# Kernel optimization log

Hardware: AMD Instinct MI355X
Metric: run time of the kernel (lower is better)

Reference implementation:

```python
import jax, jax.numpy as jnp
import numpy as np

N_NODES = 100000
N_EDGES = 1600000
DIN = 128
DH = 128
EPS = 1e-5


def _gcn_conv(x, src, dst, W, b, n):
    # x: [N, F_in] -> [N, F_out]; PyG GCNConv: transform, add self-loops,
    # symmetric normalization D^-1/2 (A+I) D^-1/2, scatter-add, + bias.
    h = x @ W.T                                        # [N, F_out]
    loops = jnp.arange(n, dtype=src.dtype)
    s = jnp.concatenate([src, loops])                  # [E+N]
    d = jnp.concatenate([dst, loops])                  # [E+N]
    w = jnp.ones(s.shape[0], dtype=x.dtype)
    deg = jax.ops.segment_sum(w, d, num_segments=n)    # [N]
    dinv = jnp.where(deg > 0, jax.lax.rsqrt(deg), 0.0)
    norm = dinv[s] * dinv[d]                           # [E+N]
    msg = h[s] * norm[:, None]                         # [E+N, F_out] (big buffer)
    out = jax.ops.segment_sum(msg, d, num_segments=n)  # [N, F_out]
    return out + b


def setup_inputs() -> dict:
    key = jax.random.key(0)
    ks = jax.random.split(key, 8)
    x = jax.random.normal(ks[0], (N_NODES, DIN), dtype=jnp.float32)
    edge_index = jax.random.randint(ks[1], (2, N_EDGES), 0, N_NODES, dtype=jnp.int32)
    sc = 1.0 / np.sqrt(DIN)
    return {
        "x": x,
        "edge_index": edge_index,
        "gamma": jnp.ones((DIN,), jnp.float32),
        "beta": jnp.zeros((DIN,), jnp.float32),
        "W1": jax.random.normal(ks[2], (DH, DIN), jnp.float32) * sc,
        "b1": jnp.zeros((DH,), jnp.float32),
        "W2": jax.random.normal(ks[3], (DH, DH), jnp.float32) * (1.0 / np.sqrt(DH)),
        "b2": jnp.zeros((DH,), jnp.float32),
        "Wc1": jax.random.normal(ks[4], (16, DH), jnp.float32) * (1.0 / np.sqrt(DH)),
        "bc1": jnp.zeros((16,), jnp.float32),
        "Wc2": jax.random.normal(ks[5], (2, 16), jnp.float32) * 0.25,
        "bc2": jnp.zeros((2,), jnp.float32),
    }


def reference(x, edge_index, gamma, beta, W1, b1, W2, b2, Wc1, bc1, Wc2, bc2):
    n = x.shape[0]
    src, dst = edge_index[0], edge_index[1]
    # BatchNorm1d (training mode: batch stats, biased variance)
    mu = jnp.mean(x, axis=0)
    var = jnp.mean((x - mu) ** 2, axis=0)
    xn = (x - mu) * jax.lax.rsqrt(var + EPS) * gamma + beta
    h = jax.nn.relu(_gcn_conv(xn, src, dst, W1, b1, n))
    h = jax.nn.relu(_gcn_conv(h, src, dst, W2, b2, n))
    h = jax.nn.relu(h @ Wc1.T + bc1)
    return h @ Wc2.T + bc2  # [N, 2]
```

## Files before the change

### kernel.cpp

```cpp
#include <hip/hip_runtime.h>
#include <hip/hip_fp16.h>

#define NFEAT 128
#define EPSV 1e-5f
#define BSH 9
#define BSZ 512
#define CHUNK 8192
#define CAP 12288

typedef _Float16 h8 __attribute__((ext_vector_type(8)));
typedef float f4 __attribute__((ext_vector_type(4)));

__global__ __launch_bounds__(256) void k_stats(const float4* __restrict__ X4,
    float* __restrict__ part, int total4)
{
    int t = threadIdx.x;
    int stride = gridDim.x * 256;
    int i = blockIdx.x * 256 + t;
    float4 s = make_float4(0.f, 0.f, 0.f, 0.f);
    float4 q = make_float4(0.f, 0.f, 0.f, 0.f);
    for (; i + 3 * stride < total4; i += 4 * stride) {
        float4 a = X4[i], b = X4[i + stride], c = X4[i + 2 * stride], d = X4[i + 3 * stride];
        s.x += (a.x + b.x) + (c.x + d.x);
        s.y += (a.y + b.y) + (c.y + d.y);
        s.z += (a.z + b.z) + (c.z + d.z);
        s.w += (a.w + b.w) + (c.w + d.w);
        q.x += (a.x * a.x + b.x * b.x) + (c.x * c.x + d.x * d.x);
        q.y += (a.y * a.y + b.y * b.y) + (c.y * c.y + d.y * d.y);
        q.z += (a.z * a.z + b.z * b.z) + (c.z * c.z + d.z * d.z);
        q.w += (a.w * a.w + b.w * b.w) + (c.w * c.w + d.w * d.w);
    }
    for (; i < total4; i += stride) {
        float4 a = X4[i];
        s.x += a.x; s.y += a.y; s.z += a.z; s.w += a.w;
        q.x = fmaf(a.x, a.x, q.x); q.y = fmaf(a.y, a.y, q.y);
        q.z = fmaf(a.z, a.z, q.z); q.w = fmaf(a.w, a.w, q.w);
    }
    __shared__ float4 ls[256], lq[256];
    ls[t] = s; lq[t] = q;
    __syncthreads();
    #pragma unroll
    for (int off = 128; off >= 32; off >>= 1) {
        if (t < off) {
            float4 a = ls[t], b = ls[t + off];
            ls[t] = make_float4(a.x + b.x, a.y + b.y, a.z + b.z, a.w + b.w);
            float4 c = lq[t], d = lq[t + off];
            lq[t] = make_float4(c.x + d.x, c.y + d.y, c.z + d.z, c.w + d.w);
        }
        __syncthreads();
    }
    if (t < 32) {
        float4* p4 = (float4*)(part + blockIdx.x * 256);
        p4[t] = ls[t];
        p4[32 + t] = lq[t];
    }
}

__global__ __launch_bounds__(256) void k_stats2(const float* __restrict__ part,
    float* __restrict__ part2)
{
    int v = threadIdx.x;
    int b0 = blockIdx.x * 32;
    float s = 0.f;
    #pragma unroll 8
    for (int j = 0; j < 32; ++j) s += part[(b0 + j) * 256 + v];
    part2[blockIdx.x * 256 + v] = s;
}

__global__ __launch_bounds__(256) void k_foldW(const float* __restrict__ W1,
    const float* __restrict__ gamma, const float* __restrict__ beta,
    const float* __restrict__ part2, float invN,
    float* __restrict__ W1p, float* __restrict__ c1)
{
    int o = (blockIdx.x * 256 + threadIdx.x) >> 6;
    int l = threadIdx.x & 63;
    float part = 0.f;
    #pragma unroll
    for (int j = 0; j < 2; ++j) {
        int k = 2 * l + j;
        float sm = 0.f, sq = 0.f;
        #pragma unroll
        for (int b = 0; b < 8; ++b) {
            sm += part2[b * 256 + k];
            sq += part2[b * 256 + 128 + k];
        }
        float mu = sm * invN;
        float var = fmaf(-mu, mu, sq * invN);
        float sc = rsqrtf(var + EPSV) * gamma[k];
        float sh = fmaf(-mu, sc, beta[k]);
        float w = W1[o * NFEAT + k];
        W1p[o * NFEAT + k] = w * sc;
        part = fmaf(sh, w, part);
    }
    #pragma unroll
    for (int off = 32; off > 0; off >>= 1) part += __shfl_down(part, off);
    if (l == 0) c1[o] = part;
}

__global__ __launch_bounds__(256) void k_bucket(const int* __restrict__ src,
    const int* __restrict__ dst, int* __restrict__ bnxt,
    int* __restrict__ packed, int E, int NB)
{
    __shared__ int hist[1024];
    __shared__ int base[1024];
    int t = threadIdx.x;
    int c0 = blockIdx.x * (CHUNK / 4);
    int c1 = min(E >> 2, c0 + CHUNK / 4);
    const int4* dst4 = (const int4*)dst;
    const int4* src4 = (const int4*)src;
    for (int i = t; i < NB; i += 256) hist[i] = 0;
    __syncthreads();
    for (int e = c0 + t; e < c1; e += 256) {
        int4 d = dst4[e];
        atomicAdd(&hist[d.x >> BSH], 1);
        atomicAdd(&hist[d.y >> BSH], 1);
        atomicAdd(&hist[d.z >> BSH], 1);
        atomicAdd(&hist[d.w >> BSH], 1);
    }
    __syncthreads();
    for (int i = t; i < NB; i += 256) {
        int h = hist[i];
        base[i] = h ? atomicAdd(&bnxt[i], h) : 0;
        hist[i] = 0;
    }
    __syncthreads();
    for (int e = c0 + t; e < c1; e += 256) {
        int4 d = dst4[e];
        int4 s = src4[e];
        int b, p;
        b = d.x >> BSH; p = base[b] + atomicAdd(&hist[b], 1); packed[b * CAP + p] = (s.x << BSH) | (d.x & (BSZ - 1));
        b = d.y >> BSH; p = base[b] + atomicAdd(&hist[b], 1); packed[b * CAP + p] = (s.y << BSH) | (d.y & (BSZ - 1));
        b = d.z >> BSH; p = base[b] + atomicAdd(&hist[b], 1); packed[b * CAP + p] = (s.z << BSH) | (d.z & (BSZ - 1));
        b = d.w >> BSH; p = base[b] + atomicAdd(&hist[b], 1); packed[b * CAP + p] = (s.w << BSH) | (d.w & (BSZ - 1));
    }
    if (blockIdx.x == 0) {
        for (int e = (E & ~3) + t; e < E; e += 256) {
            int d = dst[e];
            int b = d >> BSH;
            int p = atomicAdd(&bnxt[b], 1);
            packed[b * CAP + p] = (src[e] << BSH) | (d & (BSZ - 1));
        }
    }
}

__global__ __launch_bounds__(256) void k_bscan(const int* __restrict__ bnxt,
    int* __restrict__ boff, int NB)
{
    __shared__ int ps[256];
    int t = threadIdx.x;
    int v = (t < NB) ? bnxt[t] : 0;
    ps[t] = v;
    __syncthreads();
    #pragma unroll
    for (int off = 1; off < 256; off <<= 1) {
        int u = ps[t];
        if (t >= off) u += ps[t - off];
        __syncthreads();
        ps[t] = u;
        __syncthreads();
    }
    if (t < NB) boff[t] = ps[t] - v;
    if (t == NB - 1) boff[NB] = ps[t];
}

__global__ __launch_bounds__(256) void k_bdp(const int* __restrict__ packed,
    const int* __restrict__ bnxt, const int* __restrict__ boff,
    int* __restrict__ rp, float* __restrict__ dinv,
    int* __restrict__ csr, int N, int E)
{
    __shared__ int cnt[BSZ];
    __shared__ int ps[256];
    int b = blockIdx.x, t = threadIdx.x;
    cnt[2 * t] = 0; cnt[2 * t + 1] = 0;
    __syncthreads();
    int ecnt = bnxt[b];
    const int* pk = packed + b * CAP;
    const int4* p4 = (const int4*)pk;
    int n4 = ecnt >> 2;
    for (int e = t; e < n4; e += 256) {
        int4 v = p4[e];
        atomicAdd(&cnt[v.x & (BSZ - 1)], 1);
        atomicAdd(&cnt[v.y & (BSZ - 1)], 1);
        atomicAdd(&cnt[v.z & (BSZ - 1)], 1);
        atomicAdd(&cnt[v.w & (BSZ - 1)], 1);
    }
    for (int e = (n4 << 2) + t; e < ecnt; e += 256)
        atomicAdd(&cnt[pk[e] & (BSZ - 1)], 1);
    __syncthreads();
    int v0 = cnt[2 * t], v1 = cnt[2 * t + 1];
    int ts = v0 + v1;
    ps[t] = ts;
    __syncthreads();
    #pragma unroll
    for (int off = 1; off < 256; off <<= 1) {
        int u = ps[t];
        if (t >= off) u += ps[t - off];
        __syncthreads();
        ps[t] = u;
        __syncthreads();
    }
    int gbase = boff[b] + ps[t] - ts;
    cnt[2 * t] = gbase;
    cnt[2 * t + 1] = gbase + v0;
    int nbase = b << BSH;
    if (nbase + 2 * t < N) {
        rp[nbase + 2 * t] = gbase;
        dinv[nbase + 2 * t] = rsqrtf((float)(v0 + 1));
    }
    if (nbase + 2 * t + 1 < N) {
        rp[nbase + 2 * t + 1] = gbase + v0;
        dinv[nbase + 2 * t + 1] = rsqrtf((float)(v1 + 1));
    }
    if (b == 0 && t == 0) rp[N] = E;
    __syncthreads();
    for (int e = t; e < n4; e += 256) {
        int4 v = p4[e];
        int p;
        p = atomicAdd(&cnt[v.x & (BSZ - 1)], 1); csr[p] = v.x >> BSH;
        p = atomicAdd(&cnt[v.y & (BSZ - 1)], 1); csr[p] = v.y >> BSH;
        p = atomicAdd(&cnt[v.z & (BSZ - 1)], 1); csr[p] = v.z >> BSH;
        p = atomicAdd(&cnt[v.w & (BSZ - 1)], 1); csr[p] = v.w >> BSH;
    }
    for (int e = (n4 << 2) + t; e < ecnt; e += 256) {
        int v = pk[e];
        int p = atomicAdd(&cnt[v & (BSZ - 1)], 1);
        csr[p] = v >> BSH;
    }
}

__global__ __launch_bounds__(256) void k_gemm_f32(const float4* __restrict__ X4,
    const float* __restrict__ W, const float* __restrict__ C,
    const float* __restrict__ dinv, _Float16* __restrict__ Y, int N)
{
    __shared__ _Float16 w16[NFEAT * 136];
    __shared__ _Float16 ost[4 * 16 * 136];
    const float4* W4 = (const float4*)W;
    for (int idx = threadIdx.x; idx < NFEAT * NFEAT / 4; idx += 256) {
        float4 w = W4[idx];
        int o = idx >> 5, k = (idx & 31) * 4;
        _Float16* d = &w16[o * 136 + k];
        d[0] = (_Float16)w.x; d[1] = (_Float16)w.y;
        d[2] = (_Float16)w.z; d[3] = (_Float16)w.w;
    }
    __syncthreads();

    const h8* Wv = (const h8*)w16;
    h8* Yv = (h8*)Y;
    int lane = threadIdx.x & 63;
    int lr = lane & 15;
    int lk = lane >> 4;
    _Float16* slab = ost + (threadIdx.x >> 6) * (16 * 136);
    h8* slabv = (h8*)slab;
    int wid = (blockIdx.x * blockDim.x + threadIdx.x) >> 6;
    int nw = (gridDim.x * blockDim.x) >> 6;
    int ntiles = N >> 4;

    for (int tile = wid; tile < ntiles; tile += nw) {
        int r0 = tile << 4;
        h8 a[4];
        #pragma unroll
        for (int kg = 0; kg < 4; ++kg) {
            long fi = (long)(r0 + lr) * 32 + (kg * 4 + lk) * 2;
            float4 u = X4[fi];
            float4 v = X4[fi + 1];
            a[kg][0] = (_Float16)u.x; a[kg][1] = (_Float16)u.y;
            a[kg][2] = (_Float16)u.z; a[kg][3] = (_Float16)u.w;
            a[kg][4] = (_Float16)v.x; a[kg][5] = (_Float16)v.y;
            a[kg][6] = (_Float16)v.z; a[kg][7] = (_Float16)v.w;
        }

        f4 acc[8];
        #pragma unroll
        for (int nt = 0; nt < 8; ++nt) acc[nt] = (f4)(0.f);
        #pragma unroll
        for (int nt = 0; nt < 8; ++nt) {
            int o = nt * 16 + lr;
            #pragma unroll
            for (int kg = 0; kg < 4; ++kg) {
                h8 b = Wv[o * 17 + kg * 4 + lk];
                acc[nt] = __builtin_amdgcn_mfma_f32_16x16x32_f16(a[kg], b, acc[nt], 0, 0, 0);
            }
        }

        int rbase = lk * 4;
        float dv0 = dinv[r0 + rbase + 0];
        float dv1 = dinv[r0 + rbase + 1];
        float dv2 = dinv[r0 + rbase + 2];
        float dv3 = dinv[r0 + rbase + 3];
        #pragma unroll
        for (int nt = 0; nt < 8; ++nt) {
            int c = nt * 16 + lr;
            float cb = C[c];
            slab[(rbase + 0) * 136 + c] = (_Float16)((acc[nt][0] + cb) * dv0);
            slab[(rbase + 1) * 136 + c] = (_Float16)((acc[nt][1] + cb) * dv1);
            slab[(rbase + 2) * 136 + c] = (_Float16)((acc[nt][2] + cb) * dv2);
            slab[(rbase + 3) * 136 + c] = (_Float16)((acc[nt][3] + cb) * dv3);
        }
        #pragma unroll
        for (int j = 0; j < 4; ++j) {
            int row = j * 4 + lk;
            Yv[(long)(r0 + row) * 16 + lr] = slabv[row * 17 + lr];
        }
    }
}

__global__ __launch_bounds__(256) void k_gemm_f16(const _Float16* __restrict__ X,
    const float* __restrict__ W, const float* __restrict__ dinv,
    _Float16* __restrict__ Y, int N)
{
    __shared__ _Float16 w16[NFEAT * 136];
    __shared__ _Float16 ost[4 * 16 * 136];
    const float4* W4 = (const float4*)W;
    for (int idx = threadIdx.x; idx < NFEAT * NFEAT / 4; idx += 256) {
        float4 w = W4[idx];
        int o = idx >> 5, k = (idx & 31) * 4;
        _Float16* d = &w16[o * 136 + k];
        d[0] = (_Float16)w.x; d[1] = (_Float16)w.y;
        d[2] = (_Float16)w.z; d[3] = (_Float16)w.w;
    }
    __syncthreads();

    const h8* Xv = (const h8*)X;
    const h8* Wv = (const h8*)w16;
    h8* Yv = (h8*)Y;
    int lane = threadIdx.x & 63;
    int lr = lane & 15;
    int lk = lane >> 4;
    _Float16* slab = ost + (threadIdx.x >> 6) * (16 * 136);
    h8* slabv = (h8*)slab;
    int wid = (blockIdx.x * blockDim.x + threadIdx.x) >> 6;
    int nw = (gridDim.x * blockDim.x) >> 6;
    int ntiles = N >> 4;

    for (int tile = wid; tile < ntiles; tile += nw) {
        int r0 = tile << 4;
        h8 a[4];
        #pragma unroll
        for (int kg = 0; kg < 4; ++kg)
            a[kg] = Xv[(long)(r0 + lr) * 16 + kg * 4 + lk];

        f4 acc[8];
        #pragma unroll
        for (int nt = 0; nt < 8; ++nt) acc[nt] = (f4)(0.f);
        #pragma unroll
        for (int nt = 0; nt < 8; ++nt) {
            int o = nt * 16 + lr;
            #pragma unroll
            for (int kg = 0; kg < 4; ++kg) {
                h8 b = Wv[o * 17 + kg * 4 + lk];
                acc[nt] = __builtin_amdgcn_mfma_f32_16x16x32_f16(a[kg], b, acc[nt], 0, 0, 0);
            }
        }

        int rbase = lk * 4;
        float dv0 = dinv[r0 + rbase + 0];
        float dv1 = dinv[r0 + rbase + 1];
        float dv2 = dinv[r0 + rbase + 2];
        float dv3 = dinv[r0 + rbase + 3];
        #pragma unroll
        for (int nt = 0; nt < 8; ++nt) {
            int c = nt * 16 + lr;
            slab[(rbase + 0) * 136 + c] = (_Float16)(acc[nt][0] * dv0);
            slab[(rbase + 1) * 136 + c] = (_Float16)(acc[nt][1] * dv1);
            slab[(rbase + 2) * 136 + c] = (_Float16)(acc[nt][2] * dv2);
            slab[(rbase + 3) * 136 + c] = (_Float16)(acc[nt][3] * dv3);
        }
        #pragma unroll
        for (int j = 0; j < 4; ++j) {
            int row = j * 4 + lk;
            Yv[(long)(r0 + row) * 16 + lr] = slabv[row * 17 + lr];
        }
    }
}

__global__ __launch_bounds__(256) void k_agg(const unsigned int* __restrict__ TT,
    const int* __restrict__ rp, const int* __restrict__ csr,
    const float* __restrict__ dinv, const float* __restrict__ bias,
    unsigned int* __restrict__ OUT, int N)
{
    int wid = (blockIdx.x * 256 + threadIdx.x) >> 6;
    if (wid >= N) return;
    int lane = threadIdx.x & 63;
    unsigned int sv = TT[wid * 64 + lane];
    float2 acc = __half22float2(*(const __half2*)&sv);
    int e = rp[wid], e1 = rp[wid + 1];
    for (; e + 16 <= e1; e += 16) {
        int si[16];
        #pragma unroll
        for (int j = 0; j < 16; ++j) si[j] = csr[e + j];
        unsigned int v[16];
        #pragma unroll
        for (int j = 0; j < 16; ++j) v[j] = TT[si[j] * 64 + lane];
        float ax = 0.f, ay = 0.f;
        #pragma unroll
        for (int j = 0; j < 16; ++j) {
            float2 f = __half22float2(*(const __half2*)&v[j]);
            ax += f.x; ay += f.y;
        }
        acc.x += ax; acc.y += ay;
    }
    for (; e + 8 <= e1; e += 8) {
        int s0 = csr[e + 0], s1 = csr[e + 1], s2 = csr[e + 2], s3 = csr[e + 3];
        int s4 = csr[e + 4], s5 = csr[e + 5], s6 = csr[e + 6], s7 = csr[e + 7];
        unsigned int v0 = TT[s0 * 64 + lane];
        unsigned int v1 = TT[s1 * 64 + lane];
        unsigned int v2 = TT[s2 * 64 + lane];
        unsigned int v3 = TT[s3 * 64 + lane];
        unsigned int v4 = TT[s4 * 64 + lane];
        unsigned int v5 = TT[s5 * 64 + lane];
        unsigned int v6 = TT[s6 * 64 + lane];
        unsigned int v7 = TT[s7 * 64 + lane];
        float2 f0 = __half22float2(*(const __half2*)&v0);
        float2 f1 = __half22float2(*(const __half2*)&v1);
        float2 f2 = __half22float2(*(const __half2*)&v2);
        float2 f3 = __half22float2(*(const __half2*)&v3);
        float2 f4_ = __half22float2(*(const __half2*)&v4);
        float2 f5 = __half22float2(*(const __half2*)&v5);
        float2 f6 = __half22float2(*(const __half2*)&v6);
        float2 f7 = __half22float2(*(const __half2*)&v7);
        acc.x += ((f0.x + f1.x) + (f2.x + f3.x)) + ((f4_.x + f5.x) + (f6.x + f7.x));
        acc.y += ((f0.y + f1.y) + (f2.y + f3.y)) + ((f4_.y + f5.y) + (f6.y + f7.y));
    }
    for (; e < e1; ++e) {
        int s = csr[e];
        unsigned int v = TT[s * 64 + lane];
        float2 f = __half22float2(*(const __half2*)&v);
        acc.x += f.x; acc.y += f.y;
    }
    float dv = dinv[wid];
    float ox = fmaxf(fmaf(acc.x, dv, bias[lane * 2 + 0]), 0.f);
    float oy = fmaxf(fmaf(acc.y, dv, bias[lane * 2 + 1]), 0.f);
    __half2 o2 = __floats2half2_rn(ox, oy);
    OUT[wid * 64 + lane] = *(unsigned int*)&o2;
}

__global__ __launch_bounds__(256) void k_head(const __half* __restrict__ H,
    const float* __restrict__ Wc1, const float* __restrict__ bc1,
    const float* __restrict__ Wc2, const float* __restrict__ bc2,
    float* __restrict__ OUT, int N)
{
    __shared__ float w1[16][132];
    __shared__ float hs[16][132];
    __shared__ float h16[16][17];
    const float4* Wc14 = (const float4*)Wc1;
    for (int idx = threadIdx.x; idx < 16 * NFEAT / 4; idx += 256) {
        float4 w = Wc14[idx];
        int o = idx >> 5, k = (idx & 31) * 4;
        w1[o][k] = w.x; w1[o][k + 1] = w.y; w1[o][k + 2] = w.z; w1[o][k + 3] = w.w;
    }
    const uint4* Hu4 = (const uint4*)H;
    int ntiles = (N + 15) >> 4;
    for (int tile = blockIdx.x; tile < ntiles; tile += gridDim.x) {
        int row0 = tile << 4;
        __syncthreads();
        {
            int r = threadIdx.x >> 4, p = threadIdx.x & 15;
            int row = row0 + r;
            uint4 v = (row < N) ? Hu4[(long)row * 16 + p] : make_uint4(0, 0, 0, 0);
            float2 f0 = __half22float2(*(const __half2*)&v.x);
            float2 f1 = __half22float2(*(const __half2*)&v.y);
            float2 f2 = __half22float2(*(const __half2*)&v.z);
            float2 f3 = __half22float2(*(const __half2*)&v.w);
            int c = p * 8;
            hs[r][c + 0] = f0.x; hs[r][c + 1] = f0.y;
            hs[r][c + 2] = f1.x; hs[r][c + 3] = f1.y;
            hs[r][c + 4] = f2.x; hs[r][c + 5] = f2.y;
            hs[r][c + 6] = f3.x; hs[r][c + 7] = f3.y;
        }
        __syncthreads();
        int r = threadIdx.x >> 4, o = threadIdx.x & 15;
        float acc = 0.f;
        #pragma unroll 8
        for (int k = 0; k < NFEAT; ++k) acc = fmaf(hs[r][k], w1[o][k], acc);
        h16[r][o] = fmaxf(acc + bc1[o], 0.f);
        __syncthreads();
        if (threadIdx.x < 32) {
            int rr = threadIdx.x >> 1, j = threadIdx.x & 1;
            float a = bc2[j];
            #pragma unroll
            for (int o2 = 0; o2 < 16; ++o2) a = fmaf(h16[rr][o2], Wc2[j * 16 + o2], a);
            int row = row0 + rr;
            if (row < N) OUT[(long)row * 2 + j] = a;
        }
        __syncthreads();
    }
}

extern "C" void kernel_launch(void* const* d_in, const int* in_sizes, int n_in,
                              void* d_out, int out_size, void* d_ws, size_t ws_size,
                              hipStream_t stream) {
    const float* x     = (const float*)d_in[0];
    const int*   ei    = (const int*)d_in[1];
    const float* gamma = (const float*)d_in[2];
    const float* beta  = (const float*)d_in[3];
    const float* W1    = (const float*)d_in[4];
    const float* b1    = (const float*)d_in[5];
    const float* W2    = (const float*)d_in[6];
    const float* b2    = (const float*)d_in[7];
    const float* Wc1   = (const float*)d_in[8];
    const float* bc1   = (const float*)d_in[9];
    const float* Wc2   = (const float*)d_in[10];
    const float* bc2   = (const float*)d_in[11];

    int N = in_sizes[0] / NFEAT;
    int E = in_sizes[1] / 2;
    const int* srcI = ei;
    const int* dstI = ei + E;
    int NB = (N + BSZ - 1) >> BSH;

    char* ws = (char*)d_ws;
    size_t off = 0;
    auto alloc = [&](size_t bytes) {
        void* p = ws + off;
        off += bytes;
        off = (off + 511) & ~(size_t)511;
        return p;
    };
    __half* bufA  = (__half*)alloc((size_t)N * NFEAT * 2);
    __half* bufB  = (__half*)alloc((size_t)N * NFEAT * 2);
    float* part   = (float*)alloc(256 * 256 * 4);
    float* part2  = (float*)alloc(8 * 256 * 4);
    float* W1p    = (float*)alloc(NFEAT * NFEAT * 4);
    float* c1     = (float*)alloc(NFEAT * 4);
    int*   rp     = (int*)alloc((size_t)(N + 1) * 4);
    float* dinv   = (float*)alloc((size_t)N * 4);
    int*   csr    = (int*)alloc((size_t)E * 4);
    int*   packed = (int*)alloc((size_t)NB * CAP * 4);
    int*   bnxt   = (int*)alloc((size_t)(NB + 1) * 4);
    int*   boff   = (int*)alloc((size_t)(NB + 1) * 4);
    (void)ws_size;

    hipMemsetAsync(bnxt, 0, (size_t)(NB + 1) * 4, stream);

    int total4 = (int)((long)N * NFEAT / 4);
    int nchunk = (E + CHUNK - 1) / CHUNK;
    int naggb = (N + 3) / 4;

    k_stats<<<256, 256, 0, stream>>>((const float4*)x, part, total4);
    k_stats2<<<8, 256, 0, stream>>>(part, part2);
    k_foldW<<<32, 256, 0, stream>>>(W1, gamma, beta, part2, 1.0f / (float)N, W1p, c1);

    k_bucket<<<nchunk, 256, 0, stream>>>(srcI, dstI, bnxt, packed, E, NB);
    k_bscan<<<1, 256, 0, stream>>>(bnxt, boff, NB);
    k_bdp<<<NB, 256, 0, stream>>>(packed, bnxt, boff, rp, dinv, csr, N, E);

    k_gemm_f32<<<512, 256, 0, stream>>>((const float4*)x, W1p, c1, dinv, (_Float16*)bufB, N);
    k_agg<<<naggb, 256, 0, stream>>>((const unsigned int*)bufB, rp, csr, dinv, b1, (unsigned int*)bufA, N);
    k_gemm_f16<<<512, 256, 0, stream>>>((const _Float16*)bufA, W2, dinv, (_Float16*)bufB, N);
    k_agg<<<naggb, 256, 0, stream>>>((const unsigned int*)bufB, rp, csr, dinv, b2, (unsigned int*)bufA, N);
    k_head<<<2048, 256, 0, stream>>>(bufA, Wc1, bc1, Wc2, bc2, (float*)d_out, N);
}
```

Measured before the change: 256.5 us.

## Fuse BN stats with edge bucketing and fold bucket scan into k_bdp

Merges the BatchNorm statistics reduction and the edge bucketing pass into one kernel launch, split by block index, so the two independent phases run concurrently on the GPU. It also removes the single-block bucket scan kernel by having every k_bdp block recompute the prefix over bucket counts in shared memory. This cuts two kernel launches and lets the memory-bound stats pass overlap with the atomic-heavy bucketing. The cost is redundant scans in each k_bdp block and higher shared memory use per block in the fused kernel, which may lower occupancy.

```diff
diff --git a/kernel.cpp b/kernel.cpp
--- a/kernel.cpp
+++ b/kernel.cpp
@@ -11,48 +11,93 @@
 typedef _Float16 h8 __attribute__((ext_vector_type(8)));
 typedef float f4 __attribute__((ext_vector_type(4)));
 
-__global__ __launch_bounds__(256) void k_stats(const float4* __restrict__ X4,
-    float* __restrict__ part, int total4)
-{
+__global__ __launch_bounds__(256) void k_front(const float4* __restrict__ X4,
+    float* __restrict__ part, int total4,
+    const int* __restrict__ src, const int* __restrict__ dst,
+    int* __restrict__ bnxt, int* __restrict__ packed, int E, int NB)
+{
+    __shared__ float4 ls[256], lq[256];
+    __shared__ int hist[1024], base[1024];
     int t = threadIdx.x;
-    int stride = gridDim.x * 256;
-    int i = blockIdx.x * 256 + t;
-    float4 s = make_float4(0.f, 0.f, 0.f, 0.f);
-    float4 q = make_float4(0.f, 0.f, 0.f, 0.f);
-    for (; i + 3 * stride < total4; i += 4 * stride) {
-        float4 a = X4[i], b = X4[i + stride], c = X4[i + 2 * stride], d = X4[i + 3 * stride];
-        s.x += (a.x + b.x) + (c.x + d.x);
-        s.y += (a.y + b.y) + (c.y + d.y);
-        s.z += (a.z + b.z) + (c.z + d.z);
-        s.w += (a.w + b.w) + (c.w + d.w);
-        q.x += (a.x * a.x + b.x * b.x) + (c.x * c.x + d.x * d.x);
-        q.y += (a.y * a.y + b.y * b.y) + (c.y * c.y + d.y * d.y);
-        q.z += (a.z * a.z + b.z * b.z) + (c.z * c.z + d.z * d.z);
-        q.w += (a.w * a.w + b.w * b.w) + (c.w * c.w + d.w * d.w);
-    }
-    for (; i < total4; i += stride) {
-        float4 a = X4[i];
-        s.x += a.x; s.y += a.y; s.z += a.z; s.w += a.w;
-        q.x = fmaf(a.x, a.x, q.x); q.y = fmaf(a.y, a.y, q.y);
-        q.z = fmaf(a.z, a.z, q.z); q.w = fmaf(a.w, a.w, q.w);
-    }
-    __shared__ float4 ls[256], lq[256];
-    ls[t] = s; lq[t] = q;
-    __syncthreads();
-    #pragma unroll
-    for (int off = 128; off >= 32; off >>= 1) {
-        if (t < off) {
-            float4 a = ls[t], b = ls[t + off];
-            ls[t] = make_float4(a.x + b.x, a.y + b.y, a.z + b.z, a.w + b.w);
-            float4 c = lq[t], d = lq[t + off];
-            lq[t] = make_float4(c.x + d.x, c.y + d.y, c.z + d.z, c.w + d.w);
-        }
-        __syncthreads();
-    }
-    if (t < 32) {
-        float4* p4 = (float4*)(part + blockIdx.x * 256);
-        p4[t] = ls[t];
-        p4[32 + t] = lq[t];
+
+    if (blockIdx.x < 256) {
+        int stride = 256 * 256;
+        int i = blockIdx.x * 256 + t;
+        float4 s = make_float4(0.f, 0.f, 0.f, 0.f);
+        float4 q = make_float4(0.f, 0.f, 0.f, 0.f);
+        for (; i + 3 * stride < total4; i += 4 * stride) {
+            float4 a = X4[i], b = X4[i + stride], c = X4[i + 2 * stride], d = X4[i + 3 * stride];
+            s.x += (a.x + b.x) + (c.x + d.x);
+            s.y += (a.y + b.y) + (c.y + d.y);
+            s.z += (a.z + b.z) + (c.z + d.z);
+            s.w += (a.w + b.w) + (c.w + d.w);
+            q.x += (a.x * a.x + b.x * b.x) + (c.x * c.x + d.x * d.x);
+            q.y += (a.y * a.y + b.y * b.y) + (c.y * c.y + d.y * d.y);
+            q.z += (a.z * a.z + b.z * b.z) + (c.z * c.z + d.z * d.z);
+            q.w += (a.w * a.w + b.w * b.w) + (c.w * c.w + d.w * d.w);
+        }
+        for (; i < total4; i += stride) {
+            float4 a = X4[i];
+            s.x += a.x; s.y += a.y; s.z += a.z; s.w += a.w;
+            q.x = fmaf(a.x, a.x, q.x); q.y = fmaf(a.y, a.y, q.y);
+            q.z = fmaf(a.z, a.z, q.z); q.w = fmaf(a.w, a.w, q.w);
+        }
+        ls[t] = s; lq[t] = q;
+        __syncthreads();
+        #pragma unroll
+        for (int off = 128; off >= 32; off >>= 1) {
+            if (t < off) {
+                float4 a = ls[t], b = ls[t + off];
+                ls[t] = make_float4(a.x + b.x, a.y + b.y, a.z + b.z, a.w + b.w);
+                float4 c = lq[t], d = lq[t + off];
+                lq[t] = make_float4(c.x + d.x, c.y + d.y, c.z + d.z, c.w + d.w);
+            }
+            __syncthreads();
+        }
+        if (t < 32) {
+            float4* p4 = (float4*)(part + blockIdx.x * 256);
+            p4[t] = ls[t];
+            p4[32 + t] = lq[t];
+        }
+    } else {
+        int cb = blockIdx.x - 256;
+        int c0 = cb * (CHUNK / 4);
+        int c1 = min(E >> 2, c0 + CHUNK / 4);
+        const int4* dst4 = (const int4*)dst;
+        const int4* src4 = (const int4*)src;
+        for (int i = t; i < NB; i += 256) hist[i] = 0;
+        __syncthreads();
+        for (int e = c0 + t; e < c1; e += 256) {
+            int4 d = dst4[e];
+            atomicAdd(&hist[d.x >> BSH], 1);
+            atomicAdd(&hist[d.y >> BSH], 1);
+            atomicAdd(&hist[d.z >> BSH], 1);
+            atomicAdd(&hist[d.w >> BSH], 1);
+        }
+        __syncthreads();
+        for (int i = t; i < NB; i += 256) {
+            int h = hist[i];
+            base[i] = h ? atomicAdd(&bnxt[i], h) : 0;
+            hist[i] = 0;
+        }
+        __syncthreads();
+        for (int e = c0 + t; e < c1; e += 256) {
+            int4 d = dst4[e];
+            int4 s = src4[e];
+            int b, p;
+            b = d.x >> BSH; p = base[b] + atomicAdd(&hist[b], 1); packed[b * CAP + p] = (s.x << BSH) | (d.x & (BSZ - 1));
+            b = d.y >> BSH; p = base[b] + atomicAdd(&hist[b], 1); packed[b * CAP + p] = (s.y << BSH) | (d.y & (BSZ - 1));
+            b = d.z >> BSH; p = base[b] + atomicAdd(&hist[b], 1); packed[b * CAP + p] = (s.z << BSH) | (d.z & (BSZ - 1));
+            b = d.w >> BSH; p = base[b] + atomicAdd(&hist[b], 1); packed[b * CAP + p] = (s.w << BSH) | (d.w & (BSZ - 1));
+        }
+        if (cb == 0) {
+            for (int e = (E & ~3) + t; e < E; e += 256) {
+                int d = dst[e];
+                int b = d >> BSH;
+                int p = atomicAdd(&bnxt[b], 1);
+                packed[b * CAP + p] = (src[e] << BSH) | (d & (BSZ - 1));
+            }
+        }
     }
 }
 
@@ -97,92 +142,38 @@
     if (l == 0) c1[o] = part;
 }
 
-__global__ __launch_bounds__(256) void k_bucket(const int* __restrict__ src,
-    const int* __restrict__ dst, int* __restrict__ bnxt,
-    int* __restrict__ packed, int E, int NB)
-{
-    __shared__ int hist[1024];
-    __shared__ int base[1024];
-    int t = threadIdx.x;
-    int c0 = blockIdx.x * (CHUNK / 4);
-    int c1 = min(E >> 2, c0 + CHUNK / 4);
-    const int4* dst4 = (const int4*)dst;
-    const int4* src4 = (const int4*)src;
-    for (int i = t; i < NB; i += 256) hist[i] = 0;
-    __syncthreads();
-    for (int e = c0 + t; e < c1; e += 256) {
-        int4 d = dst4[e];
-        atomicAdd(&hist[d.x >> BSH], 1);
-        atomicAdd(&hist[d.y >> BSH], 1);
-        atomicAdd(&hist[d.z >> BSH], 1);
-        atomicAdd(&hist[d.w >> BSH], 1);
-    }
-    __syncthreads();
-    for (int i = t; i < NB; i += 256) {
-        int h = hist[i];
-        base[i] = h ? atomicAdd(&bnxt[i], h) : 0;
-        hist[i] = 0;
-    }
-    __syncthreads();
-    for (int e = c0 + t; e < c1; e += 256) {
-        int4 d = dst4[e];
-        int4 s = src4[e];
-        int b, p;
-        b = d.x >> BSH; p = base[b] + atomicAdd(&hist[b], 1); packed[b * CAP + p] = (s.x << BSH) | (d.x & (BSZ - 1));
-        b = d.y >> BSH; p = base[b] + atomicAdd(&hist[b], 1); packed[b * CAP + p] = (s.y << BSH) | (d.y & (BSZ - 1));
-        b = d.z >> BSH; p = base[b] + atomicAdd(&hist[b], 1); packed[b * CAP + p] = (s.z << BSH) | (d.z & (BSZ - 1));
-        b = d.w >> BSH; p = base[b] + atomicAdd(&hist[b], 1); packed[b * CAP + p] = (s.w << BSH) | (d.w & (BSZ - 1));
-    }
-    if (blockIdx.x == 0) {
-        for (int e = (E & ~3) + t; e < E; e += 256) {
-            int d = dst[e];
-            int b = d >> BSH;
-            int p = atomicAdd(&bnxt[b], 1);
-            packed[b * CAP + p] = (src[e] << BSH) | (d & (BSZ - 1));
-        }
-    }
-}
-
-__global__ __launch_bounds__(256) void k_bscan(const int* __restrict__ bnxt,
-    int* __restrict__ boff, int NB)
-{
+__global__ __launch_bounds__(256) void k_bdp(const int* __restrict__ packed,
+    const int* __restrict__ bnxt,
+    int* __restrict__ rp, float* __restrict__ dinv,
+    int* __restrict__ csr, int N, int E, int NB)
+{
+    __shared__ int cnt[BSZ];
     __shared__ int ps[256];
-    int t = threadIdx.x;
+    __shared__ int pb[256];
+    int b = blockIdx.x, t = threadIdx.x;
+    cnt[2 * t] = 0; cnt[2 * t + 1] = 0;
     int v = (t < NB) ? bnxt[t] : 0;
-    ps[t] = v;
+    pb[t] = v;
     __syncthreads();
     #pragma unroll
     for (int off = 1; off < 256; off <<= 1) {
-        int u = ps[t];
-        if (t >= off) u += ps[t - off];
-        __syncthreads();
-        ps[t] = u;
-        __syncthreads();
-    }
-    if (t < NB) boff[t] = ps[t] - v;
-    if (t == NB - 1) boff[NB] = ps[t];
-}
-
-__global__ __launch_bounds__(256) void k_bdp(const int* __restrict__ packed,
-    const int* __restrict__ bnxt, const int* __restrict__ boff,
-    int* __restrict__ rp, float* __restrict__ dinv,
-    int* __restrict__ csr, int N, int E)
-{
-    __shared__ int cnt[BSZ];
-    __shared__ int ps[256];
-    int b = blockIdx.x, t = threadIdx.x;
-    cnt[2 * t] = 0; cnt[2 * t + 1] = 0;
-    __syncthreads();
+        int u = pb[t];
+        if (t >= off) u += pb[t - off];
+        __syncthreads();
+        pb[t] = u;
+        __syncthreads();
+    }
+    int boffb = (b == 0) ? 0 : pb[b - 1];
     int ecnt = bnxt[b];
     const int* pk = packed + b * CAP;
     const int4* p4 = (const int4*)pk;
     int n4 = ecnt >> 2;
     for (int e = t; e < n4; e += 256) {
-        int4 v = p4[e];
-        atomicAdd(&cnt[v.x & (BSZ - 1)], 1);
-        atomicAdd(&cnt[v.y & (BSZ - 1)], 1);
-        atomicAdd(&cnt[v.z & (BSZ - 1)], 1);
-        atomicAdd(&cnt[v.w & (BSZ - 1)], 1);
+        int4 w = p4[e];
+        atomicAdd(&cnt[w.x & (BSZ - 1)], 1);
+        atomicAdd(&cnt[w.y & (BSZ - 1)], 1);
+        atomicAdd(&cnt[w.z & (BSZ - 1)], 1);
+        atomicAdd(&cnt[w.w & (BSZ - 1)], 1);
     }
     for (int e = (n4 << 2) + t; e < ecnt; e += 256)
         atomicAdd(&cnt[pk[e] & (BSZ - 1)], 1);
@@ -199,7 +190,7 @@
         ps[t] = u;
         __syncthreads();
     }
-    int gbase = boff[b] + ps[t] - ts;
+    int gbase = boffb + ps[t] - ts;
     cnt[2 * t] = gbase;
     cnt[2 * t + 1] = gbase + v0;
     int nbase = b << BSH;
@@ -214,17 +205,17 @@
     if (b == 0 && t == 0) rp[N] = E;
     __syncthreads();
     for (int e = t; e < n4; e += 256) {
-        int4 v = p4[e];
+        int4 w = p4[e];
         int p;
-        p = atomicAdd(&cnt[v.x & (BSZ - 1)], 1); csr[p] = v.x >> BSH;
-        p = atomicAdd(&cnt[v.y & (BSZ - 1)], 1); csr[p] = v.y >> BSH;
-        p = atomicAdd(&cnt[v.z & (BSZ - 1)], 1); csr[p] = v.z >> BSH;
-        p = atomicAdd(&cnt[v.w & (BSZ - 1)], 1); csr[p] = v.w >> BSH;
+        p = atomicAdd(&cnt[w.x & (BSZ - 1)], 1); csr[p] = w.x >> BSH;
+        p = atomicAdd(&cnt[w.y & (BSZ - 1)], 1); csr[p] = w.y >> BSH;
+        p = atomicAdd(&cnt[w.z & (BSZ - 1)], 1); csr[p] = w.z >> BSH;
+        p = atomicAdd(&cnt[w.w & (BSZ - 1)], 1); csr[p] = w.w >> BSH;
     }
     for (int e = (n4 << 2) + t; e < ecnt; e += 256) {
-        int v = pk[e];
-        int p = atomicAdd(&cnt[v & (BSZ - 1)], 1);
-        csr[p] = v >> BSH;
+        int w = pk[e];
+        int p = atomicAdd(&cnt[w & (BSZ - 1)], 1);
+        csr[p] = w >> BSH;
     }
 }
 
@@ -527,7 +518,6 @@
     int*   csr    = (int*)alloc((size_t)E * 4);
     int*   packed = (int*)alloc((size_t)NB * CAP * 4);
     int*   bnxt   = (int*)alloc((size_t)(NB + 1) * 4);
-    int*   boff   = (int*)alloc((size_t)(NB + 1) * 4);
     (void)ws_size;
 
     hipMemsetAsync(bnxt, 0, (size_t)(NB + 1) * 4, stream);
@@ -536,13 +526,11 @@
     int nchunk = (E + CHUNK - 1) / CHUNK;
     int naggb = (N + 3) / 4;
 
-    k_stats<<<256, 256, 0, stream>>>((const float4*)x, part, total4);
+    k_front<<<256 + nchunk, 256, 0, stream>>>((const float4*)x, part, total4,
+                                              srcI, dstI, bnxt, packed, E, NB);
     k_stats2<<<8, 256, 0, stream>>>(part, part2);
     k_foldW<<<32, 256, 0, stream>>>(W1, gamma, beta, part2, 1.0f / (float)N, W1p, c1);
-
-    k_bucket<<<nchunk, 256, 0, stream>>>(srcI, dstI, bnxt, packed, E, NB);
-    k_bscan<<<1, 256, 0, stream>>>(bnxt, boff, NB);
-    k_bdp<<<NB, 256, 0, stream>>>(packed, bnxt, boff, rp, dinv, csr, N, E);
+    k_bdp<<<NB, 256, 0, stream>>>(packed, bnxt, rp, dinv, csr, N, E, NB);
 
     k_gemm_f32<<<512, 256, 0, stream>>>((const float4*)x, W1p, c1, dinv, (_Float16*)bufB, N);
     k_agg<<<naggb, 256, 0, stream>>>((const unsigned int*)bufB, rp, csr, dinv, b1, (unsigned int*)bufA, N);
```

Result: faster. 250.1 us (median of 2 runs) (-2.5%).
